# Optimization experiments

Hardware: AMD Instinct MI355X
Metric: run time of the kernel (lower is better)

## Reference

```python
import jax, jax.numpy as jnp
import numpy as np

Kk = 4; B = 32768; Nn = 10; F_IN = 3; F_H = 16; F_OUT = 8; HOPS = 3


def _tagconv(x, row, col, norm, W, b, n):
    # TAGConv: out = sum_k A_norm^k x W_k + b  (W: [HOPS+1, in, out])
    out = x @ W[0]
    h = x
    for k in range(1, W.shape[0]):
        h = jax.ops.segment_sum(h[row] * norm[:, None], col, num_segments=n)
        out = out + h @ W[k]
    return out + b


def setup_inputs() -> dict:
    key = jax.random.key(0)
    ks = jax.random.split(key, 8)
    G = Kk * B
    totN = G * Nn
    E1 = Nn * (Nn - 1)
    # fully-connected (no self loop) edge pattern per 10-node graph, offset per graph
    i = jnp.repeat(jnp.arange(Nn), Nn); j = jnp.tile(jnp.arange(Nn), Nn)
    m = i != j
    sl = i[m]; dl = j[m]                      # [90]
    off = (jnp.arange(G) * Nn)[:, None]
    edge_index = jnp.stack([(off + sl[None, :]).reshape(-1),
                            (off + dl[None, :]).reshape(-1)], 0)
    x = jax.random.normal(ks[0], (totN, F_IN), jnp.float32)
    edge_weight = jax.random.uniform(ks[1], (G * E1,), jnp.float32)
    eigen = jax.random.uniform(ks[2], (G,), jnp.float32)
    a_0 = jnp.ones((1,), jnp.float32)
    W0 = jax.random.normal(ks[3], (HOPS + 1, F_IN, F_H), jnp.float32) / np.sqrt(F_IN)
    b0 = jnp.zeros((F_H,), jnp.float32)
    W1 = jax.random.normal(ks[4], (HOPS + 1, F_H, F_OUT), jnp.float32) / np.sqrt(F_H)
    b1 = jnp.zeros((F_OUT,), jnp.float32)
    bp_w = jax.random.normal(ks[5], (F_OUT,), jnp.float32) / np.sqrt(F_OUT)
    cp_w = jax.random.normal(ks[6], (F_OUT,), jnp.float32) / np.sqrt(F_OUT)
    w_w = jax.random.normal(ks[7], (F_OUT, F_OUT), jnp.float32) / np.sqrt(F_OUT)
    return {"x": x, "edge_index": edge_index, "edge_weight": edge_weight,
            "K": Kk, "batch_size": B, "N": Nn, "eigen": eigen, "a_0": a_0,
            "W0": W0, "b0": b0, "W1": W1, "b1": b1,
            "bp_w": bp_w, "cp_w": cp_w, "w_w": w_w}


def reference(x, edge_index, edge_weight, K, batch_size, N, eigen, a_0,
              W0, b0, W1, b1, bp_w, cp_w, w_w):
    totN = x.shape[0]
    G = K * batch_size
    E1 = N * (N - 1)
    row, col = edge_index[0], edge_index[1]
    # --- vectorized replacement of the K*batch loop over to_dense_adj ---
    w_kbe = edge_weight.reshape(K, batch_size, E1)
    src = edge_index[0, :E1]
    dst = edge_index[1, :E1]
    R = jnp.zeros((K, batch_size, N, N), x.dtype).at[:, :, src, dst].add(w_kbe)
    R = R * eigen.reshape(K, batch_size)[:, :, None, None]
    # --- GCN symmetric norm (no self loops), as in PyG TAGConv ---
    deg = jax.ops.segment_sum(edge_weight, col, num_segments=totN)
    dinv = jnp.where(deg > 0, deg ** -0.5, 0.0).astype(x.dtype)
    norm = dinv[row] * edge_weight * dinv[col]
    y = jax.nn.leaky_relu(_tagconv(x, row, col, norm, W0, b0, totN))
    y = jax.nn.leaky_relu(_tagconv(y, row, col, norm, W1, b1, totN))
    a_y = y @ bp_w            # [totN]
    t_y = y @ cp_w            # [totN]
    yw = (y @ w_w.T).reshape(G, N, -1)
    yb = y.reshape(G, N, -1)
    K_y = jnp.einsum('gnd,gmd->gnm', yw, yb).reshape(K, batch_size, N, N)
    k_ij = jax.nn.softmax(K_y, axis=0)   # softmax over the K states axis
    path_mod = jnp.maximum(x[:, 2], 0.0).reshape(G, N)
    a_ik = (a_0[0] + jax.nn.relu(a_y)).reshape(K, batch_size, N)
    t_k = t_y.reshape(G, N) * (1.0 - path_mod)
    t_k = jnp.where(t_k == 0.0, jnp.asarray(-1e10, t_k.dtype), t_k)
    t_j = jax.nn.softmax(t_k.reshape(K, batch_size, N), axis=0)
    R_t = jnp.swapaxes(R, 2, 3)
    return (k_ij, a_ik, t_j, R, R_t)
```

## Files before the change

### kernel.cpp

```cpp
#include <hip/hip_runtime.h>

#define KK 4
#define BATCH 32768
#define NN 10
#define GPW 6
#define SLAB 132
#define NTHREADS 256

static constexpr size_t OFF_AIK = (size_t)KK * BATCH * NN * NN;
static constexpr size_t OFF_TJ  = OFF_AIK + (size_t)KK * BATCH * NN;
static constexpr size_t OFF_R   = OFF_TJ  + (size_t)KK * BATCH * NN;
static constexpr size_t OFF_RT  = OFF_R   + (size_t)KK * BATCH * NN * NN;

#define WSYNC() do { asm volatile("" ::: "memory"); \
                     __builtin_amdgcn_wave_barrier(); \
                     asm volatile("" ::: "memory"); } while (0)

__device__ __forceinline__ float rcpf(float x) {
#if __has_builtin(__builtin_amdgcn_rcpf)
    return __builtin_amdgcn_rcpf(x);
#else
    return 1.f / x;
#endif
}
__device__ __forceinline__ float fexp2(float x) {
#if __has_builtin(__builtin_amdgcn_exp2f)
    return __builtin_amdgcn_exp2f(x);
#else
    return exp2f(x);
#endif
}

static __device__ __forceinline__ float2 pk_mul2(float2 a, float2 b) {
    float2 d; asm("v_pk_mul_f32 %0, %1, %2" : "=v"(d) : "v"(a), "v"(b)); return d; }
static __device__ __forceinline__ float2 pk_fma2(float2 a, float2 b, float2 c) {
    float2 d; asm("v_pk_fma_f32 %0, %1, %2, %3" : "=v"(d) : "v"(a), "v"(b), "v"(c)); return d; }
static __device__ __forceinline__ float2 pk_fma_blo(float2 a, float2 b, float2 c) {
    float2 d; asm("v_pk_fma_f32 %0, %1, %2, %3 op_sel_hi:[0,1,1]"
                  : "=v"(d) : "v"(a), "v"(b), "v"(c)); return d; }
static __device__ __forceinline__ float2 pk_fma_bhi(float2 a, float2 b, float2 c) {
    float2 d; asm("v_pk_fma_f32 %0, %1, %2, %3 op_sel:[1,0,0] op_sel_hi:[1,1,1]"
                  : "=v"(d) : "v"(a), "v"(b), "v"(c)); return d; }
static __device__ __forceinline__ float2 pk_fma_blo_s(float2 a, float2 bs, float2 c) {
    float2 d; asm("v_pk_fma_f32 %0, %1, %2, %3 op_sel_hi:[0,1,1]"
                  : "=v"(d) : "v"(a), "s"(bs), "v"(c)); return d; }
static __device__ __forceinline__ float2 pk_fma_bhi_s(float2 a, float2 bs, float2 c) {
    float2 d; asm("v_pk_fma_f32 %0, %1, %2, %3 op_sel:[1,0,0] op_sel_hi:[1,1,1]"
                  : "=v"(d) : "v"(a), "s"(bs), "v"(c)); return d; }
static __device__ __forceinline__ float2 pk_mul_blo_s(float2 a, float2 bs) {
    float2 d; asm("v_pk_mul_f32 %0, %1, %2 op_sel_hi:[0,1]"
                  : "=v"(d) : "v"(a), "s"(bs)); return d; }
static __device__ __forceinline__ float2 pk_fma_vs(float2 a, float2 bs, float2 c) {
    float2 d; asm("v_pk_fma_f32 %0, %1, %2, %3" : "=v"(d) : "v"(a), "s"(bs), "v"(c)); return d; }
static __device__ __forceinline__ float2 pk_add_vs(float2 a, float2 bs) {
    float2 d; asm("v_pk_add_f32 %0, %1, %2" : "=v"(d) : "v"(a), "s"(bs)); return d; }
static __device__ __forceinline__ float2 el_max2(float2 a, float2 b) {
    return make_float2(fmaxf(a.x, b.x), fmaxf(a.y, b.y)); }
static __device__ __forceinline__ float2 leaky2(float2 v) {
    return make_float2(fmaxf(v.x, 0.f) + 0.01f * fminf(v.x, 0.f),
                       fmaxf(v.y, 0.f) + 0.01f * fminf(v.y, 0.f)); }

__global__ __launch_bounds__(NTHREADS, 8)
void gnn_fused(const float* __restrict__ xin,
               const float* __restrict__ ew,
               const float* __restrict__ eigen,
               const float* __restrict__ a0p,
               const float* __restrict__ W0p,
               const float* __restrict__ b0p,
               const float* __restrict__ W1p,
               const float* __restrict__ b1p,
               const float* __restrict__ bpp,
               const float* __restrict__ cpp,
               const float* __restrict__ wwp,
               float* __restrict__ out)
{
    __shared__ __align__(16) float sm[KK * GPW * SLAB];

    const float LOG2E = 1.4426950408889634f;

    const int t = threadIdx.x;
    const int l = t & 63;
    const int w = t >> 6;
    int s = l / 10;
    const int n = l % 10;
    const bool dup = (s >= GPW);
    if (dup) s = GPW - 1;
    const int bb  = blockIdx.x * GPW + s;
    const bool valid = (!dup) && (bb < BATCH);
    const int bbc = (bb < BATCH) ? bb : (BATCH - 1);
    const int g   = w * BATCH + bbc;

    float* slab = sm + (w * GPW + s) * SLAB;

    float rowv[9];
    {
        const float* rp = ew + (size_t)g * 90 + n * 9;
#pragma unroll
        for (int c = 0; c < 9; ++c) rowv[c] = rp[c];
    }
    const size_t node = (size_t)g * NN + n;
    const float x0 = xin[node * 3 + 0];
    const float x1 = xin[node * 3 + 1];
    const float x2 = xin[node * 3 + 2];
    const float eig = eigen[g];
    const float a0v = a0p[0];

    float wout[10];
    wout[0] = (n == 0) ? 0.f : rowv[0];
    wout[9] = (n == 9) ? 0.f : rowv[8];
#pragma unroll
    for (int j = 1; j < 9; ++j)
        wout[j] = (j == n) ? 0.f : ((j < n) ? rowv[j] : rowv[j - 1]);

    if (valid) {
        float* pr = out + OFF_R + (size_t)g * 100 + n * 10;
#pragma unroll
        for (int q = 0; q < 5; ++q)
            ((float2*)pr)[q] = make_float2(wout[2*q] * eig, wout[2*q+1] * eig);
    }

#pragma unroll
    for (int j = 0; j < 10; ++j) slab[j * 10 + n] = wout[j];
    WSYNC();
    float2 win2[5];
    {
        const float* rp = slab + n * 10;
#pragma unroll
        for (int q = 0; q < 5; ++q) win2[q] = *(const float2*)(rp + 2 * q);
    }
    const float deg = (win2[0].x + win2[0].y) + (win2[1].x + win2[1].y)
                    + (win2[2].x + win2[2].y) + (win2[3].x + win2[3].y)
                    + (win2[4].x + win2[4].y);

    if (valid) {
        float* pt = out + OFF_RT + (size_t)g * 100 + n * 10;
#pragma unroll
        for (int q = 0; q < 5; ++q)
            ((float2*)pt)[q] = make_float2(win2[q].x * eig, win2[q].y * eig);
    }

    const float dv = (deg > 0.f) ? __frsqrt_rn(deg) : 0.f;
    slab[120 + n] = dv;
    WSYNC();
    float2 dinv2[5];
#pragma unroll
    for (int q = 0; q < 5; ++q) dinv2[q] = *(const float2*)(slab + 120 + 2 * q);
    const float2 dv2 = make_float2(dv, dv);
    float2 arow2[5];
#pragma unroll
    for (int q = 0; q < 5; ++q)
        arow2[q] = pk_mul2(pk_mul2(dinv2[q], win2[q]), dv2);

    const float2 x01 = make_float2(x0, x1);
    const float2 x2p = make_float2(x2, 0.f);
    float2 acc0p[8];
#pragma unroll
    for (int q = 0; q < 8; ++q) {
        float2 wa = *(const float2*)(W0p + 2*q);
        float2 wb = *(const float2*)(W0p + 16 + 2*q);
        float2 wc = *(const float2*)(W0p + 32 + 2*q);
        acc0p[q] = pk_mul_blo_s(x01, wa);
        acc0p[q] = pk_fma_bhi_s(x01, wb, acc0p[q]);
        acc0p[q] = pk_fma_blo_s(x2p, wc, acc0p[q]);
    }
    {
        float2 hab = x01, hcj = x2p;
#pragma unroll
        for (int hop = 1; hop <= 3; ++hop) {
            *(float4*)(slab + n * 12) = make_float4(hab.x, hab.y, hcj.x, hcj.y);
            WSYNC();
            float2 nab = make_float2(0.f, 0.f), ncj = make_float2(0.f, 0.f);
#pragma unroll
            for (int m = 0; m < 10; ++m) {
                const float4 hm = *(const float4*)(slab + m * 12);
                const float2 hx = make_float2(hm.x, hm.y);
                const float2 hz = make_float2(hm.z, hm.w);
                const float2 am = arow2[m >> 1];
                if ((m & 1) == 0) {
                    nab = pk_fma_blo(am, hx, nab);
                    ncj = pk_fma_blo(am, hz, ncj);
                } else {
                    nab = pk_fma_bhi(am, hx, nab);
                    ncj = pk_fma_bhi(am, hz, ncj);
                }
            }
            WSYNC();
#pragma unroll
            for (int q = 0; q < 8; ++q) {
                float2 wa = *(const float2*)(W0p + hop*48 + 2*q);
                float2 wb = *(const float2*)(W0p + hop*48 + 16 + 2*q);
                float2 wc = *(const float2*)(W0p + hop*48 + 32 + 2*q);
                acc0p[q] = pk_fma_blo_s(nab, wa, acc0p[q]);
                acc0p[q] = pk_fma_bhi_s(nab, wb, acc0p[q]);
                acc0p[q] = pk_fma_blo_s(ncj, wc, acc0p[q]);
            }
            hab = nab; hcj = ncj;
        }
    }
    const float2 zero2 = make_float2(0.f, 0.f);
    float2 y1p[8];
#pragma unroll
    for (int q = 0; q < 8; ++q) {
        float2 b2 = *(const float2*)(b0p + 2*q);
        y1p[q] = leaky2(pk_add_vs(acc0p[q], b2));
    }

    float2 cur2[4];
#pragma unroll
    for (int q = 0; q < 4; ++q) {
        float2 w0 = *(const float2*)(W1p + 384 + 2*q);
        cur2[q] = pk_mul_blo_s(y1p[0], w0);
        float2 w1 = *(const float2*)(W1p + 384 + 8 + 2*q);
        cur2[q] = pk_fma_bhi_s(y1p[0], w1, cur2[q]);
#pragma unroll
        for (int p8 = 1; p8 < 8; ++p8) {
            float2 wl = *(const float2*)(W1p + 384 + (2*p8)*8 + 2*q);
            float2 wh = *(const float2*)(W1p + 384 + (2*p8+1)*8 + 2*q);
            cur2[q] = pk_fma_blo_s(y1p[p8], wl, cur2[q]);
            cur2[q] = pk_fma_bhi_s(y1p[p8], wh, cur2[q]);
        }
    }
#pragma unroll
    for (int kh = 2; kh >= 0; --kh) {
        *(float4*)(slab + n * 12)     = make_float4(cur2[0].x, cur2[0].y, cur2[1].x, cur2[1].y);
        *(float4*)(slab + n * 12 + 4) = make_float4(cur2[2].x, cur2[2].y, cur2[3].x, cur2[3].y);
        WSYNC();
        float2 ag[4] = {zero2, zero2, zero2, zero2};
#pragma unroll
        for (int m = 0; m < 10; ++m) {
            const float4 p = *(const float4*)(slab + m * 12);
            const float4 r = *(const float4*)(slab + m * 12 + 4);
            const float2 pa = make_float2(p.x, p.y), pb = make_float2(p.z, p.w);
            const float2 ra = make_float2(r.x, r.y), rb = make_float2(r.z, r.w);
            const float2 am = arow2[m >> 1];
            if ((m & 1) == 0) {
                ag[0] = pk_fma_blo(am, pa, ag[0]);
                ag[1] = pk_fma_blo(am, pb, ag[1]);
                ag[2] = pk_fma_blo(am, ra, ag[2]);
                ag[3] = pk_fma_blo(am, rb, ag[3]);
            } else {
                ag[0] = pk_fma_bhi(am, pa, ag[0]);
                ag[1] = pk_fma_bhi(am, pb, ag[1]);
                ag[2] = pk_fma_bhi(am, ra, ag[2]);
                ag[3] = pk_fma_bhi(am, rb, ag[3]);
            }
        }
        WSYNC();
#pragma unroll
        for (int q = 0; q < 4; ++q) {
            cur2[q] = ag[q];
#pragma unroll
            for (int p8 = 0; p8 < 8; ++p8) {
                float2 wl = *(const float2*)(W1p + kh*128 + (2*p8)*8 + 2*q);
                float2 wh = *(const float2*)(W1p + kh*128 + (2*p8+1)*8 + 2*q);
                cur2[q] = pk_fma_blo_s(y1p[p8], wl, cur2[q]);
                cur2[q] = pk_fma_bhi_s(y1p[p8], wh, cur2[q]);
            }
        }
    }
    float2 y2p[4];
#pragma unroll
    for (int q = 0; q < 4; ++q) {
        float2 b2 = *(const float2*)(b1p + 2*q);
        y2p[q] = leaky2(pk_add_vs(cur2[q], b2));
    }

    *(float4*)(slab + n * 12)     = make_float4(y2p[0].x, y2p[0].y, y2p[1].x, y2p[1].y);
    *(float4*)(slab + n * 12 + 4) = make_float4(y2p[2].x, y2p[2].y, y2p[3].x, y2p[3].y);

    float2 accA = zero2, accT = zero2;
#pragma unroll
    for (int q = 0; q < 4; ++q) {
        float2 bp2 = *(const float2*)(bpp + 2*q);
        float2 cp2 = *(const float2*)(cpp + 2*q);
        accA = pk_fma_vs(y2p[q], bp2, accA);
        accT = pk_fma_vs(y2p[q], cp2, accT);
    }
    const float ay = accA.x + accA.y;
    const float ty = accT.x + accT.y;
    if (valid)
        out[OFF_AIK + (size_t)g * 10 + n] = a0v + fmaxf(ay, 0.f);

    float tk = ty * (1.f - fmaxf(x2, 0.f));
    if (tk == 0.f) tk = -1e10f;
    const float tks = tk * LOG2E;

    float2 yw2[4];
#pragma unroll
    for (int qd = 0; qd < 4; ++qd) {
        float2 aA = zero2, aB = zero2;
#pragma unroll
        for (int q = 0; q < 4; ++q) {
            float2 wA = *(const float2*)(wwp + (2*qd)*8 + 2*q);
            float2 wB = *(const float2*)(wwp + (2*qd+1)*8 + 2*q);
            aA = pk_fma_vs(y2p[q], wA, aA);
            aB = pk_fma_vs(y2p[q], wB, aB);
        }
        yw2[qd] = make_float2(aA.x + aA.y, aB.x + aB.y);
    }
    WSYNC();
    float kyr[10];
#pragma unroll
    for (int m = 0; m < 10; ++m) {
        const float4 p = *(const float4*)(slab + m * 12);
        const float4 r = *(const float4*)(slab + m * 12 + 4);
        float2 acc = pk_mul2(yw2[0], make_float2(p.x, p.y));
        acc = pk_fma2(yw2[1], make_float2(p.z, p.w), acc);
        acc = pk_fma2(yw2[2], make_float2(r.x, r.y), acc);
        acc = pk_fma2(yw2[3], make_float2(r.z, r.w), acc);
        kyr[m] = (acc.x + acc.y) * LOG2E;
    }
    WSYNC();
#pragma unroll
    for (int q = 0; q < 5; ++q)
        *(float2*)(slab + n * 10 + 2*q) = make_float2(kyr[2*q], kyr[2*q+1]);
    slab[120 + n] = tks;

    __syncthreads();

    {
        const float tv0 = sm[(0*GPW + s)*SLAB + 120 + n];
        const float tv1 = sm[(1*GPW + s)*SLAB + 120 + n];
        const float tv2 = sm[(2*GPW + s)*SLAB + 120 + n];
        const float tv3 = sm[(3*GPW + s)*SLAB + 120 + n];
        const float mx = fmaxf(fmaxf(tv0, tv1), fmaxf(tv2, tv3));
        const float e0 = fexp2(tv0-mx), e1 = fexp2(tv1-mx);
        const float e2 = fexp2(tv2-mx), e3 = fexp2(tv3-mx);
        const float den = e0 + e1 + e2 + e3;
        const float own = (w == 0) ? e0 : (w == 1) ? e1 : (w == 2) ? e2 : e3;
        if (valid)
            out[OFF_TJ + (size_t)g * 10 + n] = own * rcpf(den);
    }
    {
        const float* k0 = sm + (0*GPW + s)*SLAB + n * 10;
        const float* k1 = sm + (1*GPW + s)*SLAB + n * 10;
        const float* k2 = sm + (2*GPW + s)*SLAB + n * 10;
        const float* k3 = sm + (3*GPW + s)*SLAB + n * 10;
        float* po = out + (size_t)g * 100 + n * 10;
#pragma unroll
        for (int q = 0; q < 5; ++q) {
            const float2 a = *(const float2*)(k0 + 2*q);
            const float2 b = *(const float2*)(k1 + 2*q);
            const float2 c = *(const float2*)(k2 + 2*q);
            const float2 d = *(const float2*)(k3 + 2*q);
            const float2 mx2v = el_max2(el_max2(a, b), el_max2(c, d));
            const float eax = fexp2(a.x-mx2v.x), ebx = fexp2(b.x-mx2v.x);
            const float ecx = fexp2(c.x-mx2v.x), edx = fexp2(d.x-mx2v.x);
            const float eay = fexp2(a.y-mx2v.y), eby = fexp2(b.y-mx2v.y);
            const float ecy = fexp2(c.y-mx2v.y), edy = fexp2(d.y-mx2v.y);
            const float dl = eax + ebx + ecx + edx;
            const float dh = eay + eby + ecy + edy;
            const float ox = (w == 0) ? eax : (w == 1) ? ebx : (w == 2) ? ecx : edx;
            const float oy = (w == 0) ? eay : (w == 1) ? eby : (w == 2) ? ecy : edy;
            if (valid)
                ((float2*)po)[q] = make_float2(ox * rcpf(dl), oy * rcpf(dh));
        }
    }
}

extern "C" void kernel_launch(void* const* d_in, const int* in_sizes, int n_in,
                              void* d_out, int out_size, void* d_ws, size_t ws_size,
                              hipStream_t stream) {
    const float* x   = (const float*)d_in[0];
    const float* ew  = (const float*)d_in[2];
    const float* eig = (const float*)d_in[6];
    const float* a0  = (const float*)d_in[7];
    const float* W0  = (const float*)d_in[8];
    const float* b0  = (const float*)d_in[9];
    const float* W1  = (const float*)d_in[10];
    const float* b1  = (const float*)d_in[11];
    const float* bpw = (const float*)d_in[12];
    const float* cpw = (const float*)d_in[13];
    const float* www = (const float*)d_in[14];
    float* out = (float*)d_out;

    const int grid = (BATCH + GPW - 1) / GPW;
    gnn_fused<<<dim3(grid), dim3(NTHREADS), 0, stream>>>(
        x, ew, eig, a0, W0, b0, W1, b1, bpw, cpw, www, out);
}
```

Baseline: 75.97 us.

## Process two nodes per lane to pack twelve graphs per wave

Each lane now handles two nodes of a graph instead of one, so a 64-lane wave covers 12 graphs (60 active lanes) instead of 6 (60 lanes). That halves the number of blocks and lets global loads and stores use wider float4/float2 accesses, and the shared-memory weight and scalar loads are amortized over twice the work. The cost is roughly double the register use per thread, which is why launch bounds drop to 4 waves per SIMD and occupancy may fall, and shared memory per block doubles.

```diff
diff --git a/kernel.cpp b/kernel.cpp
--- a/kernel.cpp
+++ b/kernel.cpp
@@ -3,7 +3,7 @@
 #define KK 4
 #define BATCH 32768
 #define NN 10
-#define GPW 6
+#define GPW 12
 #define SLAB 132
 #define NTHREADS 256
 
@@ -54,13 +54,11 @@
     float2 d; asm("v_pk_fma_f32 %0, %1, %2, %3" : "=v"(d) : "v"(a), "s"(bs), "v"(c)); return d; }
 static __device__ __forceinline__ float2 pk_add_vs(float2 a, float2 bs) {
     float2 d; asm("v_pk_add_f32 %0, %1, %2" : "=v"(d) : "v"(a), "s"(bs)); return d; }
-static __device__ __forceinline__ float2 el_max2(float2 a, float2 b) {
-    return make_float2(fmaxf(a.x, b.x), fmaxf(a.y, b.y)); }
 static __device__ __forceinline__ float2 leaky2(float2 v) {
     return make_float2(fmaxf(v.x, 0.f) + 0.01f * fminf(v.x, 0.f),
                        fmaxf(v.y, 0.f) + 0.01f * fminf(v.y, 0.f)); }
 
-__global__ __launch_bounds__(NTHREADS, 8)
+__global__ __launch_bounds__(NTHREADS, 4)
 void gnn_fused(const float* __restrict__ xin,
                const float* __restrict__ ew,
                const float* __restrict__ eigen,
@@ -77,283 +75,373 @@
     __shared__ __align__(16) float sm[KK * GPW * SLAB];
 
     const float LOG2E = 1.4426950408889634f;
+    const float2 zero2 = make_float2(0.f, 0.f);
 
     const int t = threadIdx.x;
     const int l = t & 63;
     const int w = t >> 6;
-    int s = l / 10;
-    const int n = l % 10;
-    const bool dup = (s >= GPW);
-    if (dup) s = GPW - 1;
-    const int bb  = blockIdx.x * GPW + s;
-    const bool valid = (!dup) && (bb < BATCH);
+    int gg = l / 5;
+    const int t5 = l - gg * 5;
+    if (gg > 11) gg = 11;
+    const int n0 = 2 * t5, n1 = n0 + 1;
+    const int bb = blockIdx.x * GPW + gg;
+    const bool valid = (l < 60) && (bb < BATCH);
     const int bbc = (bb < BATCH) ? bb : (BATCH - 1);
     const int g   = w * BATCH + bbc;
 
-    float* slab = sm + (w * GPW + s) * SLAB;
-
-    float rowv[9];
-    {
-        const float* rp = ew + (size_t)g * 90 + n * 9;
-#pragma unroll
-        for (int c = 0; c < 9; ++c) rowv[c] = rp[c];
-    }
-    const size_t node = (size_t)g * NN + n;
-    const float x0 = xin[node * 3 + 0];
-    const float x1 = xin[node * 3 + 1];
-    const float x2 = xin[node * 3 + 2];
+    float* slab = sm + (w * GPW + gg) * SLAB;
+
+    float rw[18];
+    {
+        const float* rp = ew + (size_t)g * 90 + n0 * 9;
+#pragma unroll
+        for (int i = 0; i < 9; ++i) {
+            float2 v = *(const float2*)(rp + 2 * i);
+            rw[2*i] = v.x; rw[2*i+1] = v.y;
+        }
+    }
+    const float* xb = xin + ((size_t)g * 10 + n0) * 3;
+    const float2 f0 = *(const float2*)(xb);
+    const float2 f1 = *(const float2*)(xb + 2);
+    const float2 f2 = *(const float2*)(xb + 4);
     const float eig = eigen[g];
     const float a0v = a0p[0];
-
-    float wout[10];
-    wout[0] = (n == 0) ? 0.f : rowv[0];
-    wout[9] = (n == 9) ? 0.f : rowv[8];
-#pragma unroll
-    for (int j = 1; j < 9; ++j)
-        wout[j] = (j == n) ? 0.f : ((j < n) ? rowv[j] : rowv[j - 1]);
+    const float2 eig2 = make_float2(eig, eig);
+
+    float wA[10], wB[10];
+#pragma unroll
+    for (int j = 0; j < 10; ++j) {
+        wA[j] = (j == n0) ? 0.f : ((j < n0) ? rw[j]     : rw[j-1]);
+        wB[j] = (j == n1) ? 0.f : ((j < n1) ? rw[9+j]   : rw[8+j]);
+    }
 
     if (valid) {
-        float* pr = out + OFF_R + (size_t)g * 100 + n * 10;
-#pragma unroll
-        for (int q = 0; q < 5; ++q)
-            ((float2*)pr)[q] = make_float2(wout[2*q] * eig, wout[2*q+1] * eig);
-    }
-
-#pragma unroll
-    for (int j = 0; j < 10; ++j) slab[j * 10 + n] = wout[j];
+        float* pr = out + OFF_R + (size_t)g * 100 + n0 * 10;
+        float2 m0 = pk_mul2(make_float2(wA[0], wA[1]), eig2);
+        float2 m1 = pk_mul2(make_float2(wA[2], wA[3]), eig2);
+        float2 m2 = pk_mul2(make_float2(wA[4], wA[5]), eig2);
+        float2 m3 = pk_mul2(make_float2(wA[6], wA[7]), eig2);
+        float2 m4 = pk_mul2(make_float2(wA[8], wA[9]), eig2);
+        float2 m5 = pk_mul2(make_float2(wB[0], wB[1]), eig2);
+        float2 m6 = pk_mul2(make_float2(wB[2], wB[3]), eig2);
+        float2 m7 = pk_mul2(make_float2(wB[4], wB[5]), eig2);
+        float2 m8 = pk_mul2(make_float2(wB[6], wB[7]), eig2);
+        float2 m9 = pk_mul2(make_float2(wB[8], wB[9]), eig2);
+        *(float4*)(pr +  0) = make_float4(m0.x, m0.y, m1.x, m1.y);
+        *(float4*)(pr +  4) = make_float4(m2.x, m2.y, m3.x, m3.y);
+        *(float4*)(pr +  8) = make_float4(m4.x, m4.y, m5.x, m5.y);
+        *(float4*)(pr + 12) = make_float4(m6.x, m6.y, m7.x, m7.y);
+        *(float4*)(pr + 16) = make_float4(m8.x, m8.y, m9.x, m9.y);
+    }
+
+#pragma unroll
+    for (int j = 0; j < 10; ++j)
+        *(float2*)(slab + j * 10 + n0) = make_float2(wA[j], wB[j]);
     WSYNC();
-    float2 win2[5];
-    {
-        const float* rp = slab + n * 10;
-#pragma unroll
-        for (int q = 0; q < 5; ++q) win2[q] = *(const float2*)(rp + 2 * q);
-    }
-    const float deg = (win2[0].x + win2[0].y) + (win2[1].x + win2[1].y)
-                    + (win2[2].x + win2[2].y) + (win2[3].x + win2[3].y)
-                    + (win2[4].x + win2[4].y);
+    float inA[10], inB[10];
+    {
+        const float* rp = slab + n0 * 10;
+#pragma unroll
+        for (int q = 0; q < 5; ++q) {
+            float4 v = *(const float4*)(rp + 4 * q);
+            const int i = 4 * q;
+            ((i+0 < 10) ? inA[i+0]   : inB[i-10])   = v.x;
+            ((i+1 < 10) ? inA[(i+1)%10] : inB[i-9]) = v.y;
+            ((i+2 < 10) ? inA[(i+2)%10] : inB[i-8]) = v.z;
+            ((i+3 < 10) ? inA[(i+3)%10] : inB[i-7]) = v.w;
+        }
+    }
+    float degA = 0.f, degB = 0.f;
+#pragma unroll
+    for (int m = 0; m < 10; ++m) { degA += inA[m]; degB += inB[m]; }
 
     if (valid) {
-        float* pt = out + OFF_RT + (size_t)g * 100 + n * 10;
-#pragma unroll
-        for (int q = 0; q < 5; ++q)
-            ((float2*)pt)[q] = make_float2(win2[q].x * eig, win2[q].y * eig);
-    }
-
-    const float dv = (deg > 0.f) ? __frsqrt_rn(deg) : 0.f;
-    slab[120 + n] = dv;
+        float* pt = out + OFF_RT + (size_t)g * 100 + n0 * 10;
+        float2 m0 = pk_mul2(make_float2(inA[0], inA[1]), eig2);
+        float2 m1 = pk_mul2(make_float2(inA[2], inA[3]), eig2);
+        float2 m2 = pk_mul2(make_float2(inA[4], inA[5]), eig2);
+        float2 m3 = pk_mul2(make_float2(inA[6], inA[7]), eig2);
+        float2 m4 = pk_mul2(make_float2(inA[8], inA[9]), eig2);
+        float2 m5 = pk_mul2(make_float2(inB[0], inB[1]), eig2);
+        float2 m6 = pk_mul2(make_float2(inB[2], inB[3]), eig2);
+        float2 m7 = pk_mul2(make_float2(inB[4], inB[5]), eig2);
+        float2 m8 = pk_mul2(make_float2(inB[6], inB[7]), eig2);
+        float2 m9 = pk_mul2(make_float2(inB[8], inB[9]), eig2);
+        *(float4*)(pt +  0) = make_float4(m0.x, m0.y, m1.x, m1.y);
+        *(float4*)(pt +  4) = make_float4(m2.x, m2.y, m3.x, m3.y);
+        *(float4*)(pt +  8) = make_float4(m4.x, m4.y, m5.x, m5.y);
+        *(float4*)(pt + 12) = make_float4(m6.x, m6.y, m7.x, m7.y);
+        *(float4*)(pt + 16) = make_float4(m8.x, m8.y, m9.x, m9.y);
+    }
+
+    const float dvA = (degA > 0.f) ? __frsqrt_rn(degA) : 0.f;
+    const float dvB = (degB > 0.f) ? __frsqrt_rn(degB) : 0.f;
+    *(float2*)(slab + 120 + n0) = make_float2(dvA, dvB);
     WSYNC();
-    float2 dinv2[5];
-#pragma unroll
-    for (int q = 0; q < 5; ++q) dinv2[q] = *(const float2*)(slab + 120 + 2 * q);
-    const float2 dv2 = make_float2(dv, dv);
-    float2 arow2[5];
-#pragma unroll
-    for (int q = 0; q < 5; ++q)
-        arow2[q] = pk_mul2(pk_mul2(dinv2[q], win2[q]), dv2);
-
-    const float2 x01 = make_float2(x0, x1);
-    const float2 x2p = make_float2(x2, 0.f);
-    float2 acc0p[8];
+    float2 arA[5], arB[5];
+    {
+        float dinv[10];
+        float4 da = *(const float4*)(slab + 120);
+        float4 db = *(const float4*)(slab + 124);
+        float2 dc = *(const float2*)(slab + 128);
+        dinv[0]=da.x; dinv[1]=da.y; dinv[2]=da.z; dinv[3]=da.w;
+        dinv[4]=db.x; dinv[5]=db.y; dinv[6]=db.z; dinv[7]=db.w;
+        dinv[8]=dc.x; dinv[9]=dc.y;
+        const float2 dvA2 = make_float2(dvA, dvA);
+        const float2 dvB2 = make_float2(dvB, dvB);
+#pragma unroll
+        for (int q = 0; q < 5; ++q) {
+            const float2 dq = make_float2(dinv[2*q], dinv[2*q+1]);
+            arA[q] = pk_mul2(pk_mul2(dq, make_float2(inA[2*q], inA[2*q+1])), dvA2);
+            arB[q] = pk_mul2(pk_mul2(dq, make_float2(inB[2*q], inB[2*q+1])), dvB2);
+        }
+    }
+
+    float2 habA = make_float2(f0.x, f0.y), hcjA = make_float2(f1.x, 0.f);
+    float2 habB = make_float2(f1.y, f2.x), hcjB = make_float2(f2.y, 0.f);
+    const float x2A = f1.x, x2B = f2.y;
+    float2 accA0[8], accB0[8];
 #pragma unroll
     for (int q = 0; q < 8; ++q) {
         float2 wa = *(const float2*)(W0p + 2*q);
         float2 wb = *(const float2*)(W0p + 16 + 2*q);
         float2 wc = *(const float2*)(W0p + 32 + 2*q);
-        acc0p[q] = pk_mul_blo_s(x01, wa);
-        acc0p[q] = pk_fma_bhi_s(x01, wb, acc0p[q]);
-        acc0p[q] = pk_fma_blo_s(x2p, wc, acc0p[q]);
-    }
-    {
-        float2 hab = x01, hcj = x2p;
-#pragma unroll
-        for (int hop = 1; hop <= 3; ++hop) {
-            *(float4*)(slab + n * 12) = make_float4(hab.x, hab.y, hcj.x, hcj.y);
-            WSYNC();
-            float2 nab = make_float2(0.f, 0.f), ncj = make_float2(0.f, 0.f);
-#pragma unroll
-            for (int m = 0; m < 10; ++m) {
-                const float4 hm = *(const float4*)(slab + m * 12);
-                const float2 hx = make_float2(hm.x, hm.y);
-                const float2 hz = make_float2(hm.z, hm.w);
-                const float2 am = arow2[m >> 1];
-                if ((m & 1) == 0) {
-                    nab = pk_fma_blo(am, hx, nab);
-                    ncj = pk_fma_blo(am, hz, ncj);
-                } else {
-                    nab = pk_fma_bhi(am, hx, nab);
-                    ncj = pk_fma_bhi(am, hz, ncj);
-                }
+        accA0[q] = pk_mul_blo_s(habA, wa);
+        accA0[q] = pk_fma_bhi_s(habA, wb, accA0[q]);
+        accA0[q] = pk_fma_blo_s(hcjA, wc, accA0[q]);
+        accB0[q] = pk_mul_blo_s(habB, wa);
+        accB0[q] = pk_fma_bhi_s(habB, wb, accB0[q]);
+        accB0[q] = pk_fma_blo_s(hcjB, wc, accB0[q]);
+    }
+#pragma unroll
+    for (int hop = 1; hop <= 3; ++hop) {
+        *(float4*)(slab + n0 * 12) = make_float4(habA.x, habA.y, hcjA.x, hcjA.y);
+        *(float4*)(slab + n1 * 12) = make_float4(habB.x, habB.y, hcjB.x, hcjB.y);
+        WSYNC();
+        float2 nabA = zero2, ncjA = zero2, nabB = zero2, ncjB = zero2;
+#pragma unroll
+        for (int m = 0; m < 10; ++m) {
+            const float4 hm = *(const float4*)(slab + m * 12);
+            const float2 hx = make_float2(hm.x, hm.y);
+            const float2 hz = make_float2(hm.z, hm.w);
+            const float2 aAm = arA[m >> 1], aBm = arB[m >> 1];
+            if ((m & 1) == 0) {
+                nabA = pk_fma_blo(aAm, hx, nabA); ncjA = pk_fma_blo(aAm, hz, ncjA);
+                nabB = pk_fma_blo(aBm, hx, nabB); ncjB = pk_fma_blo(aBm, hz, ncjB);
+            } else {
+                nabA = pk_fma_bhi(aAm, hx, nabA); ncjA = pk_fma_bhi(aAm, hz, ncjA);
+                nabB = pk_fma_bhi(aBm, hx, nabB); ncjB = pk_fma_bhi(aBm, hz, ncjB);
             }
-            WSYNC();
-#pragma unroll
-            for (int q = 0; q < 8; ++q) {
-                float2 wa = *(const float2*)(W0p + hop*48 + 2*q);
-                float2 wb = *(const float2*)(W0p + hop*48 + 16 + 2*q);
-                float2 wc = *(const float2*)(W0p + hop*48 + 32 + 2*q);
-                acc0p[q] = pk_fma_blo_s(nab, wa, acc0p[q]);
-                acc0p[q] = pk_fma_bhi_s(nab, wb, acc0p[q]);
-                acc0p[q] = pk_fma_blo_s(ncj, wc, acc0p[q]);
-            }
-            hab = nab; hcj = ncj;
-        }
-    }
-    const float2 zero2 = make_float2(0.f, 0.f);
-    float2 y1p[8];
+        }
+        WSYNC();
+#pragma unroll
+        for (int q = 0; q < 8; ++q) {
+            float2 wa = *(const float2*)(W0p + hop*48 + 2*q);
+            float2 wb = *(const float2*)(W0p + hop*48 + 16 + 2*q);
+            float2 wc = *(const float2*)(W0p + hop*48 + 32 + 2*q);
+            accA0[q] = pk_fma_blo_s(nabA, wa, accA0[q]);
+            accA0[q] = pk_fma_bhi_s(nabA, wb, accA0[q]);
+            accA0[q] = pk_fma_blo_s(ncjA, wc, accA0[q]);
+            accB0[q] = pk_fma_blo_s(nabB, wa, accB0[q]);
+            accB0[q] = pk_fma_bhi_s(nabB, wb, accB0[q]);
+            accB0[q] = pk_fma_blo_s(ncjB, wc, accB0[q]);
+        }
+        habA = nabA; hcjA = ncjA; habB = nabB; hcjB = ncjB;
+    }
+    float2 y1A[8], y1B[8];
 #pragma unroll
     for (int q = 0; q < 8; ++q) {
         float2 b2 = *(const float2*)(b0p + 2*q);
-        y1p[q] = leaky2(pk_add_vs(acc0p[q], b2));
-    }
-
-    float2 cur2[4];
+        y1A[q] = leaky2(pk_add_vs(accA0[q], b2));
+        y1B[q] = leaky2(pk_add_vs(accB0[q], b2));
+    }
+
+    float2 curA[4], curB[4];
 #pragma unroll
     for (int q = 0; q < 4; ++q) {
         float2 w0 = *(const float2*)(W1p + 384 + 2*q);
-        cur2[q] = pk_mul_blo_s(y1p[0], w0);
+        curA[q] = pk_mul_blo_s(y1A[0], w0);
+        curB[q] = pk_mul_blo_s(y1B[0], w0);
         float2 w1 = *(const float2*)(W1p + 384 + 8 + 2*q);
-        cur2[q] = pk_fma_bhi_s(y1p[0], w1, cur2[q]);
+        curA[q] = pk_fma_bhi_s(y1A[0], w1, curA[q]);
+        curB[q] = pk_fma_bhi_s(y1B[0], w1, curB[q]);
 #pragma unroll
         for (int p8 = 1; p8 < 8; ++p8) {
             float2 wl = *(const float2*)(W1p + 384 + (2*p8)*8 + 2*q);
             float2 wh = *(const float2*)(W1p + 384 + (2*p8+1)*8 + 2*q);
-            cur2[q] = pk_fma_blo_s(y1p[p8], wl, cur2[q]);
-            cur2[q] = pk_fma_bhi_s(y1p[p8], wh, cur2[q]);
+            curA[q] = pk_fma_blo_s(y1A[p8], wl, curA[q]);
+            curA[q] = pk_fma_bhi_s(y1A[p8], wh, curA[q]);
+            curB[q] = pk_fma_blo_s(y1B[p8], wl, curB[q]);
+            curB[q] = pk_fma_bhi_s(y1B[p8], wh, curB[q]);
         }
     }
 #pragma unroll
     for (int kh = 2; kh >= 0; --kh) {
-        *(float4*)(slab + n * 12)     = make_float4(cur2[0].x, cur2[0].y, cur2[1].x, cur2[1].y);
-        *(float4*)(slab + n * 12 + 4) = make_float4(cur2[2].x, cur2[2].y, cur2[3].x, cur2[3].y);
+        *(float4*)(slab + n0 * 12)     = make_float4(curA[0].x, curA[0].y, curA[1].x, curA[1].y);
+        *(float4*)(slab + n0 * 12 + 4) = make_float4(curA[2].x, curA[2].y, curA[3].x, curA[3].y);
+        *(float4*)(slab + n1 * 12)     = make_float4(curB[0].x, curB[0].y, curB[1].x, curB[1].y);
+        *(float4*)(slab + n1 * 12 + 4) = make_float4(curB[2].x, curB[2].y, curB[3].x, curB[3].y);
         WSYNC();
-        float2 ag[4] = {zero2, zero2, zero2, zero2};
+        float2 agA[4] = {zero2, zero2, zero2, zero2};
+        float2 agB[4] = {zero2, zero2, zero2, zero2};
 #pragma unroll
         for (int m = 0; m < 10; ++m) {
             const float4 p = *(const float4*)(slab + m * 12);
             const float4 r = *(const float4*)(slab + m * 12 + 4);
             const float2 pa = make_float2(p.x, p.y), pb = make_float2(p.z, p.w);
             const float2 ra = make_float2(r.x, r.y), rb = make_float2(r.z, r.w);
-            const float2 am = arow2[m >> 1];
+            const float2 aAm = arA[m >> 1], aBm = arB[m >> 1];
             if ((m & 1) == 0) {
-                ag[0] = pk_fma_blo(am, pa, ag[0]);
-                ag[1] = pk_fma_blo(am, pb, ag[1]);
-                ag[2] = pk_fma_blo(am, ra, ag[2]);
-                ag[3] = pk_fma_blo(am, rb, ag[3]);
+                agA[0] = pk_fma_blo(aAm, pa, agA[0]); agA[1] = pk_fma_blo(aAm, pb, agA[1]);
+                agA[2] = pk_fma_blo(aAm, ra, agA[2]); agA[3] = pk_fma_blo(aAm, rb, agA[3]);
+                agB[0] = pk_fma_blo(aBm, pa, agB[0]); agB[1] = pk_fma_blo(aBm, pb, agB[1]);
+                agB[2] = pk_fma_blo(aBm, ra, agB[2]); agB[3] = pk_fma_blo(aBm, rb, agB[3]);
             } else {
-                ag[0] = pk_fma_bhi(am, pa, ag[0]);
-                ag[1] = pk_fma_bhi(am, pb, ag[1]);
-                ag[2] = pk_fma_bhi(am, ra, ag[2]);
-                ag[3] = pk_fma_bhi(am, rb, ag[3]);
+                agA[0] = pk_fma_bhi(aAm, pa, agA[0]); agA[1] = pk_fma_bhi(aAm, pb, agA[1]);
+                agA[2] = pk_fma_bhi(aAm, ra, agA[2]); agA[3] = pk_fma_bhi(aAm, rb, agA[3]);
+                agB[0] = pk_fma_bhi(aBm, pa, agB[0]); agB[1] = pk_fma_bhi(aBm, pb, agB[1]);
+                agB[2] = pk_fma_bhi(aBm, ra, agB[2]); agB[3] = pk_fma_bhi(aBm, rb, agB[3]);
             }
         }
         WSYNC();
 #pragma unroll
         for (int q = 0; q < 4; ++q) {
-            cur2[q] = ag[q];
+            curA[q] = agA[q]; curB[q] = agB[q];
 #pragma unroll
             for (int p8 = 0; p8 < 8; ++p8) {
                 float2 wl = *(const float2*)(W1p + kh*128 + (2*p8)*8 + 2*q);
                 float2 wh = *(const float2*)(W1p + kh*128 + (2*p8+1)*8 + 2*q);
-                cur2[q] = pk_fma_blo_s(y1p[p8], wl, cur2[q]);
-                cur2[q] = pk_fma_bhi_s(y1p[p8], wh, cur2[q]);
+                curA[q] = pk_fma_blo_s(y1A[p8], wl, curA[q]);
+                curA[q] = pk_fma_bhi_s(y1A[p8], wh, curA[q]);
+                curB[q] = pk_fma_blo_s(y1B[p8], wl, curB[q]);
+                curB[q] = pk_fma_bhi_s(y1B[p8], wh, curB[q]);
             }
         }
     }
-    float2 y2p[4];
+    float2 y2A[4], y2B[4];
 #pragma unroll
     for (int q = 0; q < 4; ++q) {
         float2 b2 = *(const float2*)(b1p + 2*q);
-        y2p[q] = leaky2(pk_add_vs(cur2[q], b2));
-    }
-
-    *(float4*)(slab + n * 12)     = make_float4(y2p[0].x, y2p[0].y, y2p[1].x, y2p[1].y);
-    *(float4*)(slab + n * 12 + 4) = make_float4(y2p[2].x, y2p[2].y, y2p[3].x, y2p[3].y);
-
-    float2 accA = zero2, accT = zero2;
+        y2A[q] = leaky2(pk_add_vs(curA[q], b2));
+        y2B[q] = leaky2(pk_add_vs(curB[q], b2));
+    }
+
+    *(float4*)(slab + n0 * 12)     = make_float4(y2A[0].x, y2A[0].y, y2A[1].x, y2A[1].y);
+    *(float4*)(slab + n0 * 12 + 4) = make_float4(y2A[2].x, y2A[2].y, y2A[3].x, y2A[3].y);
+    *(float4*)(slab + n1 * 12)     = make_float4(y2B[0].x, y2B[0].y, y2B[1].x, y2B[1].y);
+    *(float4*)(slab + n1 * 12 + 4) = make_float4(y2B[2].x, y2B[2].y, y2B[3].x, y2B[3].y);
+
+    float2 aaA = zero2, aaB = zero2, ttA = zero2, ttB = zero2;
 #pragma unroll
     for (int q = 0; q < 4; ++q) {
         float2 bp2 = *(const float2*)(bpp + 2*q);
         float2 cp2 = *(const float2*)(cpp + 2*q);
-        accA = pk_fma_vs(y2p[q], bp2, accA);
-        accT = pk_fma_vs(y2p[q], cp2, accT);
-    }
-    const float ay = accA.x + accA.y;
-    const float ty = accT.x + accT.y;
+        aaA = pk_fma_vs(y2A[q], bp2, aaA);
+        aaB = pk_fma_vs(y2B[q], bp2, aaB);
+        ttA = pk_fma_vs(y2A[q], cp2, ttA);
+        ttB = pk_fma_vs(y2B[q], cp2, ttB);
+    }
     if (valid)
-        out[OFF_AIK + (size_t)g * 10 + n] = a0v + fmaxf(ay, 0.f);
-
-    float tk = ty * (1.f - fmaxf(x2, 0.f));
-    if (tk == 0.f) tk = -1e10f;
-    const float tks = tk * LOG2E;
-
-    float2 yw2[4];
+        *(float2*)(out + OFF_AIK + (size_t)g * 10 + n0) =
+            make_float2(a0v + fmaxf(aaA.x + aaA.y, 0.f), a0v + fmaxf(aaB.x + aaB.y, 0.f));
+
+    float tkA = (ttA.x + ttA.y) * (1.f - fmaxf(x2A, 0.f));
+    float tkB = (ttB.x + ttB.y) * (1.f - fmaxf(x2B, 0.f));
+    if (tkA == 0.f) tkA = -1e10f;
+    if (tkB == 0.f) tkB = -1e10f;
+    const float2 tks = make_float2(tkA * LOG2E, tkB * LOG2E);
+
+    float2 ywA[4], ywB[4];
 #pragma unroll
     for (int qd = 0; qd < 4; ++qd) {
-        float2 aA = zero2, aB = zero2;
+        float2 aLA = zero2, aHA = zero2, aLB = zero2, aHB = zero2;
 #pragma unroll
         for (int q = 0; q < 4; ++q) {
-            float2 wA = *(const float2*)(wwp + (2*qd)*8 + 2*q);
-            float2 wB = *(const float2*)(wwp + (2*qd+1)*8 + 2*q);
-            aA = pk_fma_vs(y2p[q], wA, aA);
-            aB = pk_fma_vs(y2p[q], wB, aB);
-        }
-        yw2[qd] = make_float2(aA.x + aA.y, aB.x + aB.y);
+            float2 wL = *(const float2*)(wwp + (2*qd)*8 + 2*q);
+            float2 wH = *(const float2*)(wwp + (2*qd+1)*8 + 2*q);
+            aLA = pk_fma_vs(y2A[q], wL, aLA);
+            aHA = pk_fma_vs(y2A[q], wH, aHA);
+            aLB = pk_fma_vs(y2B[q], wL, aLB);
+            aHB = pk_fma_vs(y2B[q], wH, aHB);
+        }
+        ywA[qd] = make_float2(aLA.x + aLA.y, aHA.x + aHA.y);
+        ywB[qd] = make_float2(aLB.x + aLB.y, aHB.x + aHB.y);
     }
     WSYNC();
-    float kyr[10];
+    float kyA[10], kyB[10];
 #pragma unroll
     for (int m = 0; m < 10; ++m) {
         const float4 p = *(const float4*)(slab + m * 12);
         const float4 r = *(const float4*)(slab + m * 12 + 4);
-        float2 acc = pk_mul2(yw2[0], make_float2(p.x, p.y));
-        acc = pk_fma2(yw2[1], make_float2(p.z, p.w), acc);
-        acc = pk_fma2(yw2[2], make_float2(r.x, r.y), acc);
-        acc = pk_fma2(yw2[3], make_float2(r.z, r.w), acc);
-        kyr[m] = (acc.x + acc.y) * LOG2E;
+        const float2 pa = make_float2(p.x, p.y), pb = make_float2(p.z, p.w);
+        const float2 ra = make_float2(r.x, r.y), rb = make_float2(r.z, r.w);
+        float2 aA = pk_mul2(ywA[0], pa);
+        aA = pk_fma2(ywA[1], pb, aA);
+        aA = pk_fma2(ywA[2], ra, aA);
+        aA = pk_fma2(ywA[3], rb, aA);
+        kyA[m] = (aA.x + aA.y) * LOG2E;
+        float2 aB = pk_mul2(ywB[0], pa);
+        aB = pk_fma2(ywB[1], pb, aB);
+        aB = pk_fma2(ywB[2], ra, aB);
+        aB = pk_fma2(ywB[3], rb, aB);
+        kyB[m] = (aB.x + aB.y) * LOG2E;
     }
     WSYNC();
-#pragma unroll
-    for (int q = 0; q < 5; ++q)
-        *(float2*)(slab + n * 10 + 2*q) = make_float2(kyr[2*q], kyr[2*q+1]);
-    slab[120 + n] = tks;
+    {
+        float* kb = slab + n0 * 10;
+        *(float4*)(kb +  0) = make_float4(kyA[0], kyA[1], kyA[2], kyA[3]);
+        *(float4*)(kb +  4) = make_float4(kyA[4], kyA[5], kyA[6], kyA[7]);
+        *(float4*)(kb +  8) = make_float4(kyA[8], kyA[9], kyB[0], kyB[1]);
+        *(float4*)(kb + 12) = make_float4(kyB[2], kyB[3], kyB[4], kyB[5]);
+        *(float4*)(kb + 16) = make_float4(kyB[6], kyB[7], kyB[8], kyB[9]);
+    }
+    *(float2*)(slab + 120 + n0) = tks;
 
     __syncthreads();
 
     {
-        const float tv0 = sm[(0*GPW + s)*SLAB + 120 + n];
-        const float tv1 = sm[(1*GPW + s)*SLAB + 120 + n];
-        const float tv2 = sm[(2*GPW + s)*SLAB + 120 + n];
-        const float tv3 = sm[(3*GPW + s)*SLAB + 120 + n];
-        const float mx = fmaxf(fmaxf(tv0, tv1), fmaxf(tv2, tv3));
-        const float e0 = fexp2(tv0-mx), e1 = fexp2(tv1-mx);
-        const float e2 = fexp2(tv2-mx), e3 = fexp2(tv3-mx);
-        const float den = e0 + e1 + e2 + e3;
-        const float own = (w == 0) ? e0 : (w == 1) ? e1 : (w == 2) ? e2 : e3;
+        const float2 v0 = *(const float2*)(sm + (0*GPW + gg)*SLAB + 120 + n0);
+        const float2 v1 = *(const float2*)(sm + (1*GPW + gg)*SLAB + 120 + n0);
+        const float2 v2 = *(const float2*)(sm + (2*GPW + gg)*SLAB + 120 + n0);
+        const float2 v3 = *(const float2*)(sm + (3*GPW + gg)*SLAB + 120 + n0);
+        const float mxA = fmaxf(fmaxf(v0.x, v1.x), fmaxf(v2.x, v3.x));
+        const float mxB = fmaxf(fmaxf(v0.y, v1.y), fmaxf(v2.y, v3.y));
+        const float e0A = fexp2(v0.x-mxA), e1A = fexp2(v1.x-mxA);
+        const float e2A = fexp2(v2.x-mxA), e3A = fexp2(v3.x-mxA);
+        const float e0B = fexp2(v0.y-mxB), e1B = fexp2(v1.y-mxB);
+        const float e2B = fexp2(v2.y-mxB), e3B = fexp2(v3.y-mxB);
+        const float dA = e0A + e1A + e2A + e3A;
+        const float dB = e0B + e1B + e2B + e3B;
+        const float oA = (w == 0) ? e0A : (w == 1) ? e1A : (w == 2) ? e2A : e3A;
+        const float oB = (w == 0) ? e0B : (w == 1) ? e1B : (w == 2) ? e2B : e3B;
         if (valid)
-            out[OFF_TJ + (size_t)g * 10 + n] = own * rcpf(den);
-    }
-    {
-        const float* k0 = sm + (0*GPW + s)*SLAB + n * 10;
-        const float* k1 = sm + (1*GPW + s)*SLAB + n * 10;
-        const float* k2 = sm + (2*GPW + s)*SLAB + n * 10;
-        const float* k3 = sm + (3*GPW + s)*SLAB + n * 10;
-        float* po = out + (size_t)g * 100 + n * 10;
+            *(float2*)(out + OFF_TJ + (size_t)g * 10 + n0) =
+                make_float2(oA * rcpf(dA), oB * rcpf(dB));
+    }
+    {
+        const float* s0 = sm + (0*GPW + gg)*SLAB + n0 * 10;
+        const float* s1 = sm + (1*GPW + gg)*SLAB + n0 * 10;
+        const float* s2 = sm + (2*GPW + gg)*SLAB + n0 * 10;
+        const float* s3 = sm + (3*GPW + gg)*SLAB + n0 * 10;
+        float* po = out + (size_t)g * 100 + n0 * 10;
 #pragma unroll
         for (int q = 0; q < 5; ++q) {
-            const float2 a = *(const float2*)(k0 + 2*q);
-            const float2 b = *(const float2*)(k1 + 2*q);
-            const float2 c = *(const float2*)(k2 + 2*q);
-            const float2 d = *(const float2*)(k3 + 2*q);
-            const float2 mx2v = el_max2(el_max2(a, b), el_max2(c, d));
-            const float eax = fexp2(a.x-mx2v.x), ebx = fexp2(b.x-mx2v.x);
-            const float ecx = fexp2(c.x-mx2v.x), edx = fexp2(d.x-mx2v.x);
-            const float eay = fexp2(a.y-mx2v.y), eby = fexp2(b.y-mx2v.y);
-            const float ecy = fexp2(c.y-mx2v.y), edy = fexp2(d.y-mx2v.y);
-            const float dl = eax + ebx + ecx + edx;
-            const float dh = eay + eby + ecy + edy;
-            const float ox = (w == 0) ? eax : (w == 1) ? ebx : (w == 2) ? ecx : edx;
-            const float oy = (w == 0) ? eay : (w == 1) ? eby : (w == 2) ? ecy : edy;
-            if (valid)
-                ((float2*)po)[q] = make_float2(ox * rcpf(dl), oy * rcpf(dh));
+            const float4 a = *(const float4*)(s0 + 4*q);
+            const float4 b = *(const float4*)(s1 + 4*q);
+            const float4 c = *(const float4*)(s2 + 4*q);
+            const float4 d = *(const float4*)(s3 + 4*q);
+            float o[4];
+#pragma unroll
+            for (int e = 0; e < 4; ++e) {
+                const float va = (&a.x)[e], vb = (&b.x)[e], vc = (&c.x)[e], vd = (&d.x)[e];
+                const float mx = fmaxf(fmaxf(va, vb), fmaxf(vc, vd));
+                const float ea = fexp2(va-mx), eb = fexp2(vb-mx);
+                const float ec = fexp2(vc-mx), ed = fexp2(vd-mx);
+                const float den = ea + eb + ec + ed;
+                const float own = (w == 0) ? ea : (w == 1) ? eb : (w == 2) ? ec : ed;
+                o[e] = own * rcpf(den);
+            }
+            if (valid) *(float4*)(po + 4*q) = make_float4(o[0], o[1], o[2], o[3]);
         }
     }
 }
```

Measured after the change: 148.5 us. +95.5%, slower.
